# Kernel tuning notes

Hardware: AMD Instinct MI355X
Metric: run time of the kernel (lower is better)

Reference implementation:

```python
import jax, jax.numpy as jnp
import numpy as np

EMBED_DIM = 16
GAMMA0 = 1.0
GAMMA = 1.0
ZETA = 1.0
INV_T = 1.0
EPS = 1e-8


def setup_inputs() -> dict:
    key = jax.random.key(0)
    z = jax.random.normal(key, (16, 131072, EMBED_DIM), dtype=jnp.float32)
    return {"z": z}


def _entropy(p):
    # H = -sum p log(p + 1e-8) over last axis
    return -(p * jnp.log(p + EPS)).sum(-1)


def reference(z):
    # L2 normalize over embed dim (torch F.normalize clamps norm at 1e-12)
    norm = jnp.linalg.norm(z, axis=-1, keepdims=True)
    z = z / jnp.maximum(norm, 1e-12)

    # soft entropy loss
    p = jax.nn.sigmoid(-4.0 * z / (EMBED_DIM ** 0.5 * INV_T))  # (..., g)
    prob = jnp.stack([p, 1.0 - p], axis=-1)                     # (..., g, 2)
    persample_entropy = _entropy(prob).sum(-1).mean()           # scalar
    avg_prob = prob.reshape(-1, EMBED_DIM, 2).mean(0)           # (g, 2)
    cb_entropy = _entropy(avg_prob).sum()                       # scalar
    entropy_penalty = GAMMA0 * persample_entropy - GAMMA * cb_entropy

    # sign quantize with straight-through estimator
    zhat = jnp.where(z > 0, 1.0, -1.0).astype(z.dtype)
    zq = z + jax.lax.stop_gradient(zhat - z)

    # bit-pack codes -> indices (fits int32 for embed_dim=16)
    basis = (2 ** jnp.arange(EMBED_DIM - 1, -1, -1, dtype=jnp.int32))
    bits = ((jax.lax.stop_gradient(zq) + 1.0) * 0.5).astype(jnp.int32)
    indices = (bits * basis).sum(-1)

    zq = zq * (1.0 / EMBED_DIM ** 0.5)
    loss = ZETA * entropy_penalty / INV_T
    return zq, loss, indices, avg_prob
```

## Files before the change

kernel.cpp:

```cpp
#include <hip/hip_runtime.h>
#include <math.h>


typedef float f32x4 __attribute__((ext_vector_type(4)));

__device__ __forceinline__ float dpp_qxor1_f(float x) {
    return __int_as_float(__builtin_amdgcn_mov_dpp(__float_as_int(x), 0xB1, 0xF, 0xF, true));
}
__device__ __forceinline__ float dpp_qxor2_f(float x) {
    return __int_as_float(__builtin_amdgcn_mov_dpp(__float_as_int(x), 0x4E, 0xF, 0xF, true));
}
__device__ __forceinline__ unsigned dpp_qxor1_u(unsigned x) {
    return (unsigned)__builtin_amdgcn_mov_dpp((int)x, 0xB1, 0xF, 0xF, true);
}
__device__ __forceinline__ unsigned dpp_qxor2_u(unsigned x) {
    return (unsigned)__builtin_amdgcn_mov_dpp((int)x, 0x4E, 0xF, 0xF, true);
}

__device__ __forceinline__ void process_quad(
    const float4 v, const int c,
    float& h_acc, float* p_acc, f32x4& o, unsigned& bits)
{
    const float C1 = -0.125f, C2 = 1.0f/64.0f, C3 = -1.0f/576.0f, C4 = 119.0f/645120.0f;
    const float D0 = -0.25f,  D1 = 1.0f/48.0f, D2 = -1.0f/480.0f, D3 = 17.0f/80640.0f;

    float vv[4] = {v.x, v.y, v.z, v.w};

    float ss = 0.f;
    #pragma unroll
    for (int j = 0; j < 4; ++j) ss = fmaf(vv[j], vv[j], ss);
    ss += dpp_qxor1_f(ss);
    ss += dpp_qxor2_f(ss);
    const float scale = rsqrtf(fmaxf(ss, 1e-24f));

    bits = 0u;
    #pragma unroll
    for (int j = 0; j < 4; ++j) {
        const float s = vv[j] * scale;
        const float t = s * s;
        const float gp = fmaf(t, fmaf(t, fmaf(t, D3, D2), D1), D0);
        p_acc[j] = fmaf(s, gp, p_acc[j]);
        const float hin = fmaf(t, fmaf(t, fmaf(t, C4, C3), C2), C1);
        h_acc = fmaf(t, hin, h_acc);

        const bool bit = vv[j] > 0.0f;
        o[j] = bit ? 0.25f : -0.25f;
        bits |= (bit ? 1u : 0u) << (15 - (4 * c + j));
    }
    bits |= dpp_qxor1_u(bits);
    bits |= dpp_qxor2_u(bits);
}

__global__ __launch_bounds__(256) void bsq_main(
    const float* __restrict__ z,
    float* __restrict__ zq,
    float* __restrict__ idx_out,
    float* __restrict__ ws_h,
    float* __restrict__ ws_p,
    long long quads)
{
    const int tid = threadIdx.x;
    const long long stride = (long long)gridDim.x * blockDim.x;
    const int c = tid & 3;

    float h_acc = 0.f;
    float p_acc[4] = {0.f, 0.f, 0.f, 0.f};

    long long q = (long long)blockIdx.x * blockDim.x + tid;

    for (; q + stride < quads; q += 2 * stride) {
        const float4 va = reinterpret_cast<const float4*>(z)[q];
        const float4 vb = reinterpret_cast<const float4*>(z)[q + stride];

        f32x4 oa, ob;
        unsigned ba, bb;
        process_quad(va, c, h_acc, p_acc, oa, ba);
        process_quad(vb, c, h_acc, p_acc, ob, bb);

        __builtin_nontemporal_store(oa, reinterpret_cast<f32x4*>(zq) + q);
        __builtin_nontemporal_store(ob, reinterpret_cast<f32x4*>(zq) + q + stride);
        if (c == 0) {
            __builtin_nontemporal_store((float)ba, idx_out + (q >> 2));
            __builtin_nontemporal_store((float)bb, idx_out + ((q + stride) >> 2));
        }
    }
    for (; q < quads; q += stride) {
        const float4 v = reinterpret_cast<const float4*>(z)[q];
        f32x4 o; unsigned b;
        process_quad(v, c, h_acc, p_acc, o, b);
        __builtin_nontemporal_store(o, reinterpret_cast<f32x4*>(zq) + q);
        if (c == 0) __builtin_nontemporal_store((float)b, idx_out + (q >> 2));
    }

    #pragma unroll
    for (int m = 32; m >= 4; m >>= 1) {
        h_acc += __shfl_xor(h_acc, m);
        #pragma unroll
        for (int j = 0; j < 4; ++j) p_acc[j] += __shfl_xor(p_acc[j], m);
    }
    h_acc += __shfl_xor(h_acc, 2);
    h_acc += __shfl_xor(h_acc, 1);

    __shared__ float sh_h[4];
    __shared__ float sh_p[4][16];
    const int wave = tid >> 6;
    const int lane = tid & 63;
    if (lane == 0) sh_h[wave] = h_acc;
    if (lane < 4) {
        #pragma unroll
        for (int j = 0; j < 4; ++j) sh_p[wave][4 * lane + j] = p_acc[j];
    }
    __syncthreads();

    if (tid == 0)
        ws_h[blockIdx.x] = sh_h[0] + sh_h[1] + sh_h[2] + sh_h[3];
    if (tid < 16)
        ws_p[(long long)tid * gridDim.x + blockIdx.x] =
            sh_p[0][tid] + sh_p[1][tid] + sh_p[2][tid] + sh_p[3][tid];
}

__global__ __launch_bounds__(1024) void bsq_final(
    const float* __restrict__ ws_h,
    const float* __restrict__ ws_p,
    float* __restrict__ loss_out,
    float* __restrict__ avgp_out,
    int nb, long long rows)
{
    const int tid  = threadIdx.x;
    const int wave = tid >> 6;
    const int lane = tid & 63;
    const double invR = 1.0 / (double)rows;
    const double LN2 = 0.6931471805599453;

    __shared__ double sh_q[16];
    __shared__ double sh_h;

    double p = 0.0;
    for (int i = lane; i < nb; i += 64)
        p += (double)ws_p[(long long)wave * nb + i];

    double h = 0.0;
    if (wave == 0)
        for (int i = lane; i < nb; i += 64)
            h += (double)ws_h[i];

    #pragma unroll
    for (int m = 32; m >= 1; m >>= 1)
        p += __shfl_xor(p, m);
    if (wave == 0) {
        #pragma unroll
        for (int m = 32; m >= 1; m >>= 1)
            h += __shfl_xor(h, m);
        if (lane == 0) sh_h = 16.0 * LN2 + h * invR;
    }
    if (lane == 0) sh_q[wave] = 0.5 + p * invR;
    __syncthreads();

    if (wave == 0) {
        const double q = (lane < 16) ? sh_q[lane] : 0.0;
        double term = 0.0;
        if (lane < 16)
            term = -(q * log(q + 1e-8) + (1.0 - q) * log((1.0 - q) + 1e-8));
        #pragma unroll
        for (int m = 32; m >= 1; m >>= 1)
            term += __shfl_xor(term, m);
        if (lane == 0)
            loss_out[0] = (float)(sh_h - term);
        if (lane < 16) {
            avgp_out[2 * lane]     = (float)sh_q[lane];
            avgp_out[2 * lane + 1] = (float)(1.0 - sh_q[lane]);
        }
    }
}

extern "C" void kernel_launch(void* const* d_in, const int* in_sizes, int n_in,
                              void* d_out, int out_size, void* d_ws, size_t ws_size,
                              hipStream_t stream) {
    const float* z = (const float*)d_in[0];
    const long long n     = in_sizes[0];
    const long long rows  = n / 16;
    const long long quads = n / 4;

    float* out   = (float*)d_out;
    float* zq    = out;
    float* loss  = out + n;
    float* idx   = out + n + 1;
    float* avgp  = out + n + 1 + rows;

    const int NB = 2048;
    float* ws_h = (float*)d_ws;
    float* ws_p = ws_h + NB;

    bsq_main<<<NB, 256, 0, stream>>>(z, zq, idx, ws_h, ws_p, quads);
    bsq_final<<<1, 1024, 0, stream>>>(ws_h, ws_p, loss, avgp, NB, rows);
}
```

Before: 67.89 us.

## Split main kernel into read/reduce pass and zq reconstruction pass from indices

After: 72.81 us. 7.3% more time.

```diff
diff --git a/kernel.cpp b/kernel.cpp
--- a/kernel.cpp
+++ b/kernel.cpp
@@ -17,9 +17,8 @@
     return (unsigned)__builtin_amdgcn_mov_dpp((int)x, 0x4E, 0xF, 0xF, true);
 }
 
-__device__ __forceinline__ void process_quad(
-    const float4 v, const int c,
-    float& h_acc, float* p_acc, f32x4& o, unsigned& bits)
+__device__ __forceinline__ unsigned process_quad(
+    const float4 v, const int c, float& h_acc, float* p_acc)
 {
     const float C1 = -0.125f, C2 = 1.0f/64.0f, C3 = -1.0f/576.0f, C4 = 119.0f/645120.0f;
     const float D0 = -0.25f,  D1 = 1.0f/48.0f, D2 = -1.0f/480.0f, D3 = 17.0f/80640.0f;
@@ -33,7 +32,7 @@
     ss += dpp_qxor2_f(ss);
     const float scale = rsqrtf(fmaxf(ss, 1e-24f));
 
-    bits = 0u;
+    unsigned bits = 0u;
     #pragma unroll
     for (int j = 0; j < 4; ++j) {
         const float s = vv[j] * scale;
@@ -42,18 +41,15 @@
         p_acc[j] = fmaf(s, gp, p_acc[j]);
         const float hin = fmaf(t, fmaf(t, fmaf(t, C4, C3), C2), C1);
         h_acc = fmaf(t, hin, h_acc);
-
-        const bool bit = vv[j] > 0.0f;
-        o[j] = bit ? 0.25f : -0.25f;
-        bits |= (bit ? 1u : 0u) << (15 - (4 * c + j));
+        bits |= (vv[j] > 0.0f ? 1u : 0u) << (15 - (4 * c + j));
     }
     bits |= dpp_qxor1_u(bits);
     bits |= dpp_qxor2_u(bits);
-}
-
-__global__ __launch_bounds__(256) void bsq_main(
+    return bits;
+}
+
+__global__ __launch_bounds__(256) void bsq_pass1(
     const float* __restrict__ z,
-    float* __restrict__ zq,
     float* __restrict__ idx_out,
     float* __restrict__ ws_h,
     float* __restrict__ ws_p,
@@ -68,28 +64,28 @@
 
     long long q = (long long)blockIdx.x * blockDim.x + tid;
 
-    for (; q + stride < quads; q += 2 * stride) {
-        const float4 va = reinterpret_cast<const float4*>(z)[q];
-        const float4 vb = reinterpret_cast<const float4*>(z)[q + stride];
-
-        f32x4 oa, ob;
-        unsigned ba, bb;
-        process_quad(va, c, h_acc, p_acc, oa, ba);
-        process_quad(vb, c, h_acc, p_acc, ob, bb);
-
-        __builtin_nontemporal_store(oa, reinterpret_cast<f32x4*>(zq) + q);
-        __builtin_nontemporal_store(ob, reinterpret_cast<f32x4*>(zq) + q + stride);
+    for (; q + 3 * stride < quads; q += 4 * stride) {
+        const float4 v0 = reinterpret_cast<const float4*>(z)[q];
+        const float4 v1 = reinterpret_cast<const float4*>(z)[q + stride];
+        const float4 v2 = reinterpret_cast<const float4*>(z)[q + 2 * stride];
+        const float4 v3 = reinterpret_cast<const float4*>(z)[q + 3 * stride];
+
+        const unsigned b0 = process_quad(v0, c, h_acc, p_acc);
+        const unsigned b1 = process_quad(v1, c, h_acc, p_acc);
+        const unsigned b2 = process_quad(v2, c, h_acc, p_acc);
+        const unsigned b3 = process_quad(v3, c, h_acc, p_acc);
+
         if (c == 0) {
-            __builtin_nontemporal_store((float)ba, idx_out + (q >> 2));
-            __builtin_nontemporal_store((float)bb, idx_out + ((q + stride) >> 2));
+            idx_out[q >> 2]                  = (float)b0;
+            idx_out[(q + stride) >> 2]       = (float)b1;
+            idx_out[(q + 2 * stride) >> 2]   = (float)b2;
+            idx_out[(q + 3 * stride) >> 2]   = (float)b3;
         }
     }
     for (; q < quads; q += stride) {
         const float4 v = reinterpret_cast<const float4*>(z)[q];
-        f32x4 o; unsigned b;
-        process_quad(v, c, h_acc, p_acc, o, b);
-        __builtin_nontemporal_store(o, reinterpret_cast<f32x4*>(zq) + q);
-        if (c == 0) __builtin_nontemporal_store((float)b, idx_out + (q >> 2));
+        const unsigned b = process_quad(v, c, h_acc, p_acc);
+        if (c == 0) idx_out[q >> 2] = (float)b;
     }
 
     #pragma unroll
@@ -117,6 +113,39 @@
     if (tid < 16)
         ws_p[(long long)tid * gridDim.x + blockIdx.x] =
             sh_p[0][tid] + sh_p[1][tid] + sh_p[2][tid] + sh_p[3][tid];
+}
+
+__global__ __launch_bounds__(256) void bsq_pass2(
+    const float* __restrict__ idx_in,
+    float* __restrict__ zq,
+    long long quads)
+{
+    const int tid = threadIdx.x;
+    const long long stride = (long long)gridDim.x * blockDim.x;
+    const int c = tid & 3;
+    const int sh = 12 - 4 * c;
+
+    long long q = (long long)blockIdx.x * blockDim.x + tid;
+    for (; q + stride < quads; q += 2 * stride) {
+        const unsigned ba = (unsigned)idx_in[q >> 2];
+        const unsigned bb = (unsigned)idx_in[(q + stride) >> 2];
+        f32x4 oa, ob;
+        #pragma unroll
+        for (int j = 0; j < 4; ++j) {
+            oa[j] = ((ba >> (sh + 3 - j)) & 1u) ? 0.25f : -0.25f;
+            ob[j] = ((bb >> (sh + 3 - j)) & 1u) ? 0.25f : -0.25f;
+        }
+        __builtin_nontemporal_store(oa, reinterpret_cast<f32x4*>(zq) + q);
+        __builtin_nontemporal_store(ob, reinterpret_cast<f32x4*>(zq) + q + stride);
+    }
+    for (; q < quads; q += stride) {
+        const unsigned b = (unsigned)idx_in[q >> 2];
+        f32x4 o;
+        #pragma unroll
+        for (int j = 0; j < 4; ++j)
+            o[j] = ((b >> (sh + 3 - j)) & 1u) ? 0.25f : -0.25f;
+        __builtin_nontemporal_store(o, reinterpret_cast<f32x4*>(zq) + q);
+    }
 }
 
 __global__ __launch_bounds__(1024) void bsq_final(
@@ -191,6 +220,7 @@
     float* ws_h = (float*)d_ws;
     float* ws_p = ws_h + NB;
 
-    bsq_main<<<NB, 256, 0, stream>>>(z, zq, idx, ws_h, ws_p, quads);
+    bsq_pass1<<<NB, 256, 0, stream>>>(z, idx, ws_h, ws_p, quads);
+    bsq_pass2<<<NB, 256, 0, stream>>>(idx, zq, quads);
     bsq_final<<<1, 1024, 0, stream>>>(ws_h, ws_p, loss, avgp, NB, rows);
 }
```
